# Optimization experiments

Measured on AMD Instinct MI355X. Metric: run time of the kernel, lower is better.

The kernel has to match this reference:

```python
import jax, jax.numpy as jnp
import numpy as np

N, E, F, H = 50000, 400000, 128, 512


def setup_inputs() -> dict:
    key = jax.random.key(0)
    k1, k2, k3 = jax.random.split(key, 3)
    x = jax.random.normal(k1, (N, F), dtype=jnp.float32)
    edge_index = jax.random.randint(k2, (2, E), 0, N, dtype=jnp.int64)
    W = jax.random.normal(k3, (H, F), dtype=jnp.float32) * 0.05  # GCNConv linear weight [out, in]
    b = jnp.zeros((H,), dtype=jnp.float32)
    alpha = jnp.full((H,), 0.25, dtype=jnp.float32)  # PReLU default init per channel
    return {"x": x, "edge_index": edge_index, "W": W, "b": b, "alpha": alpha}


def reference(x, edge_index, W, b, alpha):
    n = x.shape[0]
    # GCNConv: linear transform first (no bias inside the matmul)
    h = x @ W.T  # [N, H]
    # add self-loops (GCNConv default add_self_loops=True)
    loops = jnp.arange(n, dtype=edge_index.dtype)
    row = jnp.concatenate([edge_index[0], loops])  # source
    col = jnp.concatenate([edge_index[1], loops])  # target
    # symmetric degree normalization: deg from edge weights (all ones) summed at targets
    deg = jax.ops.segment_sum(jnp.ones_like(col, dtype=h.dtype), col, num_segments=n)
    dinv = jnp.where(deg > 0, jax.lax.rsqrt(jnp.maximum(deg, 1.0)) * (deg > 0), 0.0)
    dinv = jnp.where(deg > 0, 1.0 / jnp.sqrt(jnp.maximum(deg, 1e-12)), 0.0)
    norm = dinv[row] * dinv[col]  # [E+N]
    # gather source features, scale, scatter-add to targets
    msgs = h[row] * norm[:, None]  # [E+N, H] -- the memory-bound gather
    out = jax.ops.segment_sum(msgs, col, num_segments=n) + b  # [N, H]
    # PReLU with per-channel alpha
    return jnp.where(out > 0, out, alpha * out)
```

## Files before the change

kernel.cpp:

```cpp
#include <hip/hip_runtime.h>


#define F_IN 128
#define H_OUT 512

typedef __bf16 bf16x8 __attribute__((ext_vector_type(8)));
typedef float  f32x4  __attribute__((ext_vector_type(4)));

__global__ __launch_bounds__(256) void prep_kernel(const float* __restrict__ W,
                                                   __bf16* __restrict__ Wb, int nw8,
                                                   const float* __restrict__ x,
                                                   __bf16* __restrict__ xs, int nx8,
                                                   const int* __restrict__ col,
                                                   unsigned* __restrict__ deg,
                                                   unsigned* __restrict__ pos, int E,
                                                   int NWB, int NXB) {
    const int b = blockIdx.x, t = threadIdx.x;
    if (b < NWB) {
        int i = b * 256 + t;
        if (i >= nw8) return;
        float4 a0 = ((const float4*)W)[i * 2];
        float4 a1 = ((const float4*)W)[i * 2 + 1];
        bf16x8 v;
        v[0] = (__bf16)a0.x; v[1] = (__bf16)a0.y; v[2] = (__bf16)a0.z; v[3] = (__bf16)a0.w;
        v[4] = (__bf16)a1.x; v[5] = (__bf16)a1.y; v[6] = (__bf16)a1.z; v[7] = (__bf16)a1.w;
        ((bf16x8*)Wb)[i] = v;
    } else if (b < NWB + NXB) {
        int i = (b - NWB) * 256 + t;
        if (i >= nx8) return;
        float4 a0 = ((const float4*)x)[i * 2];
        float4 a1 = ((const float4*)x)[i * 2 + 1];
        bf16x8 v;
        v[0] = (__bf16)a0.x; v[1] = (__bf16)a0.y; v[2] = (__bf16)a0.z; v[3] = (__bf16)a0.w;
        v[4] = (__bf16)a1.x; v[5] = (__bf16)a1.y; v[6] = (__bf16)a1.z; v[7] = (__bf16)a1.w;
        ((bf16x8*)xs)[i] = v;
    } else {
        int e = (b - NWB - NXB) * 256 + t;
        if (e < E) pos[e] = atomicAdd(&deg[col[e]], 1u);
    }
}

__global__ __launch_bounds__(256) void assign_kernel(const unsigned* __restrict__ deg,
                                                     unsigned* __restrict__ total,
                                                     int* __restrict__ rowptr,
                                                     float* __restrict__ dinv, int n) {
    const int i = blockIdx.x * 256 + threadIdx.x;
    const int lane = threadIdx.x & 63;
    unsigned d = (i < n) ? deg[i] : 0u;
    unsigned da = (d + 7u) & ~7u;
    unsigned x = da;
    #pragma unroll
    for (int o = 1; o < 64; o <<= 1) {
        unsigned y = __shfl_up(x, (unsigned)o, 64);
        if (lane >= o) x += y;
    }
    unsigned tot = __shfl(x, 63, 64);
    unsigned wb = 0;
    if (lane == 63) wb = atomicAdd(total, tot);
    wb = __shfl(wb, 63, 64);
    if (i < n) {
        rowptr[i] = (int)(wb + x - da);
        dinv[i]   = rsqrtf((float)(d + 1u));
    }
}

__global__ __launch_bounds__(256) void fill_csr_kernel(const int* __restrict__ row,
                                                       const int* __restrict__ col,
                                                       const unsigned* __restrict__ pos,
                                                       const int* __restrict__ rowptr,
                                                       int* __restrict__ adj, int E) {
    int e = blockIdx.x * 256 + threadIdx.x;
    if (e >= E) return;
    adj[rowptr[col[e]] + (int)pos[e]] = row[e];
}

__global__ __launch_bounds__(256) void fused_agg_gemm_kernel(
        const int* __restrict__ rowptr, const unsigned* __restrict__ deg,
        const int* __restrict__ adj, const __bf16* __restrict__ xs,
        const float* __restrict__ dinv, const __bf16* __restrict__ Wb,
        const float* __restrict__ bias, const float* __restrict__ alpha,
        float* __restrict__ out, int N) {
    __shared__ __bf16 As[128][136];
    __shared__ __bf16 Bs[128][136];

    const int rb = blockIdx.x * 128;
    const int t  = threadIdx.x;
    const int li   = t & 15;
    const int slot = t >> 4;

    const bf16x8* xs8 = (const bf16x8*)xs;

    for (int nl = slot; nl < 128; nl += 16) {
        const int node = rb + nl;
        bf16x8 o;
        if (node < N) {
            const float dvn = dinv[node];
            bf16x8 sv = xs8[(size_t)node * 16 + li];
            float acc[8];
            #pragma unroll
            for (int q = 0; q < 8; ++q) acc[q] = dvn * (float)sv[q];

            const int s = rowptr[node];
            const int e = s + (int)deg[node];
            for (int j = s; j < e; j += 8) {
                int4 ra = *(const int4*)(adj + j);
                int4 rb4 = *(const int4*)(adj + j + 4);
                int rr[8];
                rr[0] = ra.x;  rr[1] = ra.y;  rr[2] = ra.z;  rr[3] = ra.w;
                rr[4] = rb4.x; rr[5] = rb4.y; rr[6] = rb4.z; rr[7] = rb4.w;
                float wgt[8]; bf16x8 v[8];
                #pragma unroll
                for (int u = 0; u < 8; ++u) {
                    const bool ok = (j + u) < e;
                    const int r = ok ? rr[u] : node;
                    wgt[u] = ok ? dinv[r] : 0.0f;
                    v[u]   = xs8[(size_t)r * 16 + li];
                }
                #pragma unroll
                for (int u = 0; u < 8; ++u) {
                    #pragma unroll
                    for (int q = 0; q < 8; ++q) acc[q] += wgt[u] * (float)v[u][q];
                }
            }
            #pragma unroll
            for (int q = 0; q < 8; ++q) o[q] = (__bf16)(acc[q] * dvn);
        } else {
            #pragma unroll
            for (int q = 0; q < 8; ++q) o[q] = (__bf16)0.0f;
        }
        *(bf16x8*)&As[nl][li * 8] = o;
    }
    __syncthreads();

    const int w    = t >> 6;
    const int lane = t & 63;
    const int lrow = lane & 15;
    const int lk   = (lane >> 4) * 8;
    const int rloc = (lane >> 4) * 4;

    bf16x8 af0[4], af1[4];
    #pragma unroll
    for (int ks = 0; ks < 4; ++ks) {
        const int k0 = ks * 32 + lk;
        af0[ks] = *(const bf16x8*)&As[w * 32 + lrow][k0];
        af1[ks] = *(const bf16x8*)&As[w * 32 + 16 + lrow][k0];
    }

    for (int ct = 0; ct < 4; ++ct) {
        const int cb = ct * 128;
        __syncthreads();
        #pragma unroll
        for (int i = 0; i < 8; ++i) {
            int c  = i * 256 + t;
            int r  = c >> 4;
            int k8 = (c & 15) * 8;
            bf16x8 v = *(const bf16x8*)(Wb + (size_t)(cb + r) * F_IN + k8);
            *(bf16x8*)&Bs[r][k8] = v;
        }
        __syncthreads();

        f32x4 acc[2][8] = {};
        #pragma unroll
        for (int ks = 0; ks < 4; ++ks) {
            const int k0 = ks * 32 + lk;
            #pragma unroll
            for (int tn = 0; tn < 8; ++tn) {
                bf16x8 bfr = *(const bf16x8*)&Bs[tn * 16 + lrow][k0];
                acc[0][tn] = __builtin_amdgcn_mfma_f32_16x16x32_bf16(af0[ks], bfr, acc[0][tn], 0, 0, 0);
                acc[1][tn] = __builtin_amdgcn_mfma_f32_16x16x32_bf16(af1[ks], bfr, acc[1][tn], 0, 0, 0);
            }
        }

        float bb[8], aa[8];
        #pragma unroll
        for (int tn = 0; tn < 8; ++tn) {
            int n = cb + tn * 16 + lrow;
            bb[tn] = bias[n];
            aa[tn] = alpha[n];
        }
        #pragma unroll
        for (int tm = 0; tm < 2; ++tm) {
            #pragma unroll
            for (int r = 0; r < 4; ++r) {
                int m = rb + w * 32 + tm * 16 + rloc + r;
                if (m >= N) continue;
                #pragma unroll
                for (int tn = 0; tn < 8; ++tn) {
                    int n = cb + tn * 16 + lrow;
                    float v = acc[tm][tn][r] + bb[tn];
                    v = v > 0.f ? v : aa[tn] * v;
                    out[(size_t)m * H_OUT + n] = v;
                }
            }
        }
    }
}

extern "C" void kernel_launch(void* const* d_in, const int* in_sizes, int n_in,
                              void* d_out, int out_size, void* d_ws, size_t ws_size,
                              hipStream_t stream) {
    const float* x     = (const float*)d_in[0];
    const int*   ei    = (const int*)d_in[1];
    const float* W     = (const float*)d_in[2];
    const float* b     = (const float*)d_in[3];
    const float* alpha = (const float*)d_in[4];
    float*       out   = (float*)d_out;

    const int N = in_sizes[0] / F_IN;
    const int E = in_sizes[1] / 2;
    const int* row = ei;
    const int* col = ei + E;

    char* wsb = (char*)d_ws;
    size_t off = 0;
    __bf16* xs = (__bf16*)(wsb + off);  off += (size_t)N * F_IN * 2;     off = (off + 63) & ~(size_t)63;
    __bf16* Wb = (__bf16*)(wsb + off);  off += (size_t)H_OUT * F_IN * 2; off = (off + 63) & ~(size_t)63;
    unsigned* deg    = (unsigned*)(wsb + off);  off += (size_t)(N + 1) * 4;
    float*    dinv   = (float*)(wsb + off);     off += (size_t)N * 4;
    int*      rowptr = (int*)(wsb + off);       off += (size_t)N * 4;
    off = (off + 63) & ~(size_t)63;
    unsigned* pos = (unsigned*)(wsb + off);     off += (size_t)E * 4;
    off = (off + 63) & ~(size_t)63;
    int* adj = (int*)(wsb + off);
    unsigned* total = deg + N;

    const int nw8 = H_OUT * F_IN / 8;
    const int nx8 = N * F_IN / 8;
    const int NWB = (nw8 + 255) / 256;
    const int NXB = (nx8 + 255) / 256;
    const int NEB = (E + 255) / 256;

    hipMemsetAsync(deg, 0, (size_t)(N + 1) * 4, stream);
    prep_kernel<<<NWB + NXB + NEB, 256, 0, stream>>>(W, Wb, nw8, x, xs, nx8,
                                                     col, deg, pos, E, NWB, NXB);
    assign_kernel<<<(N + 255) / 256, 256, 0, stream>>>(deg, total, rowptr, dinv, N);
    fill_csr_kernel<<<(E + 255) / 256, 256, 0, stream>>>(row, col, pos, rowptr, adj, E);
    fused_agg_gemm_kernel<<<(N + 127) / 128, 256, 0, stream>>>(
        rowptr, deg, adj, xs, dinv, Wb, b, alpha, out, N);
}
```

Before: 213.3 us.

## Shrink fused agg-GEMM tile to 64 rows, drop LDS weight staging

Halves the rows per block in the fused aggregation+GEMM kernel to 64, launching twice as many blocks. It removes the shared-memory B tile, so weight fragments are read straight from global memory (L2-resident), and that removes the per-column-tile barriers. It also adds a launch bound of 3 blocks per SM and unrolls the loops, all aimed at higher occupancy to hide gather latency. The trade-off is redundant global/L2 weight reads per wave and less MFMA reuse of each B fragment.

```diff
diff --git a/kernel.cpp b/kernel.cpp
--- a/kernel.cpp
+++ b/kernel.cpp
@@ -74,23 +74,23 @@
     adj[rowptr[col[e]] + (int)pos[e]] = row[e];
 }
 
-__global__ __launch_bounds__(256) void fused_agg_gemm_kernel(
+__global__ __launch_bounds__(256, 3) void fused_agg_gemm_kernel(
         const int* __restrict__ rowptr, const unsigned* __restrict__ deg,
         const int* __restrict__ adj, const __bf16* __restrict__ xs,
         const float* __restrict__ dinv, const __bf16* __restrict__ Wb,
         const float* __restrict__ bias, const float* __restrict__ alpha,
         float* __restrict__ out, int N) {
-    __shared__ __bf16 As[128][136];
-    __shared__ __bf16 Bs[128][136];
-
-    const int rb = blockIdx.x * 128;
+    __shared__ __bf16 As[64][136];
+
+    const int rb = blockIdx.x * 64;
     const int t  = threadIdx.x;
     const int li   = t & 15;
     const int slot = t >> 4;
 
     const bf16x8* xs8 = (const bf16x8*)xs;
 
-    for (int nl = slot; nl < 128; nl += 16) {
+    #pragma unroll
+    for (int nl = slot; nl < 64; nl += 16) {
         const int node = rb + nl;
         bf16x8 o;
         if (node < N) {
@@ -103,7 +103,7 @@
             const int s = rowptr[node];
             const int e = s + (int)deg[node];
             for (int j = s; j < e; j += 8) {
-                int4 ra = *(const int4*)(adj + j);
+                int4 ra  = *(const int4*)(adj + j);
                 int4 rb4 = *(const int4*)(adj + j + 4);
                 int rr[8];
                 rr[0] = ra.x;  rr[1] = ra.y;  rr[2] = ra.z;  rr[3] = ra.w;
@@ -138,36 +138,23 @@
     const int lk   = (lane >> 4) * 8;
     const int rloc = (lane >> 4) * 4;
 
-    bf16x8 af0[4], af1[4];
-    #pragma unroll
-    for (int ks = 0; ks < 4; ++ks) {
-        const int k0 = ks * 32 + lk;
-        af0[ks] = *(const bf16x8*)&As[w * 32 + lrow][k0];
-        af1[ks] = *(const bf16x8*)&As[w * 32 + 16 + lrow][k0];
-    }
-
+    bf16x8 af[4];
+    #pragma unroll
+    for (int ks = 0; ks < 4; ++ks)
+        af[ks] = *(const bf16x8*)&As[w * 16 + lrow][ks * 32 + lk];
+
+    #pragma unroll
     for (int ct = 0; ct < 4; ++ct) {
         const int cb = ct * 128;
-        __syncthreads();
-        #pragma unroll
-        for (int i = 0; i < 8; ++i) {
-            int c  = i * 256 + t;
-            int r  = c >> 4;
-            int k8 = (c & 15) * 8;
-            bf16x8 v = *(const bf16x8*)(Wb + (size_t)(cb + r) * F_IN + k8);
-            *(bf16x8*)&Bs[r][k8] = v;
-        }
-        __syncthreads();
-
-        f32x4 acc[2][8] = {};
+
+        f32x4 acc[8] = {};
         #pragma unroll
         for (int ks = 0; ks < 4; ++ks) {
             const int k0 = ks * 32 + lk;
             #pragma unroll
             for (int tn = 0; tn < 8; ++tn) {
-                bf16x8 bfr = *(const bf16x8*)&Bs[tn * 16 + lrow][k0];
-                acc[0][tn] = __builtin_amdgcn_mfma_f32_16x16x32_bf16(af0[ks], bfr, acc[0][tn], 0, 0, 0);
-                acc[1][tn] = __builtin_amdgcn_mfma_f32_16x16x32_bf16(af1[ks], bfr, acc[1][tn], 0, 0, 0);
+                bf16x8 bfr = *(const bf16x8*)(Wb + (size_t)(cb + tn * 16 + lrow) * F_IN + k0);
+                acc[tn] = __builtin_amdgcn_mfma_f32_16x16x32_bf16(af[ks], bfr, acc[tn], 0, 0, 0);
             }
         }
 
@@ -179,18 +166,15 @@
             aa[tn] = alpha[n];
         }
         #pragma unroll
-        for (int tm = 0; tm < 2; ++tm) {
-            #pragma unroll
-            for (int r = 0; r < 4; ++r) {
-                int m = rb + w * 32 + tm * 16 + rloc + r;
-                if (m >= N) continue;
-                #pragma unroll
-                for (int tn = 0; tn < 8; ++tn) {
-                    int n = cb + tn * 16 + lrow;
-                    float v = acc[tm][tn][r] + bb[tn];
-                    v = v > 0.f ? v : aa[tn] * v;
-                    out[(size_t)m * H_OUT + n] = v;
-                }
+        for (int r = 0; r < 4; ++r) {
+            int m = rb + w * 16 + rloc + r;
+            if (m >= N) continue;
+            #pragma unroll
+            for (int tn = 0; tn < 8; ++tn) {
+                int n = cb + tn * 16 + lrow;
+                float v = acc[tn][r] + bb[tn];
+                v = v > 0.f ? v : aa[tn] * v;
+                out[(size_t)m * H_OUT + n] = v;
             }
         }
     }
@@ -235,6 +219,6 @@
                                                      col, deg, pos, E, NWB, NXB);
     assign_kernel<<<(N + 255) / 256, 256, 0, stream>>>(deg, total, rowptr, dinv, N);
     fill_csr_kernel<<<(E + 255) / 256, 256, 0, stream>>>(row, col, pos, rowptr, adj, E);
-    fused_agg_gemm_kernel<<<(N + 127) / 128, 256, 0, stream>>>(
+    fused_agg_gemm_kernel<<<(N + 63) / 64, 256, 0, stream>>>(
         rowptr, deg, adj, xs, dinv, Wb, b, alpha, out, N);
 }
```

Result: slower. 246.8 us (+15.7%).

## Split gather and GEMM into producer/consumer blocks with atomic flag handoff

Applied to the files above, without the earlier changes.

The fused kernel is split into many small gather blocks (16 nodes each) that write aggregated bf16 features to a global buffer, followed by GEMM blocks that spin on per-128-row completion counters before running MFMA. The goal is finer-grained parallelism for the irregular gather and overlap between gather and GEMM phases inside one launch. The GEMM now uses 64-column W tiles with smaller LDS, launch_bounds occupancy 4, and nontemporal output stores. It adds a global round trip for aggregated features and relies on dispatch order for the spin-wait to avoid deadlock.

```diff
diff --git a/kernel.cpp b/kernel.cpp
--- a/kernel.cpp
+++ b/kernel.cpp
@@ -74,26 +74,23 @@
     adj[rowptr[col[e]] + (int)pos[e]] = row[e];
 }
 
-__global__ __launch_bounds__(256) void fused_agg_gemm_kernel(
+__global__ __launch_bounds__(256, 4) void gather_gemm_kernel(
         const int* __restrict__ rowptr, const unsigned* __restrict__ deg,
         const int* __restrict__ adj, const __bf16* __restrict__ xs,
-        const float* __restrict__ dinv, const __bf16* __restrict__ Wb,
-        const float* __restrict__ bias, const float* __restrict__ alpha,
-        float* __restrict__ out, int N) {
-    __shared__ __bf16 As[128][136];
-    __shared__ __bf16 Bs[128][136];
-
-    const int rb = blockIdx.x * 128;
-    const int t  = threadIdx.x;
-    const int li   = t & 15;
-    const int slot = t >> 4;
-
-    const bf16x8* xs8 = (const bf16x8*)xs;
-
-    for (int nl = slot; nl < 128; nl += 16) {
-        const int node = rb + nl;
-        bf16x8 o;
+        const float* __restrict__ dinv, __bf16* __restrict__ ag,
+        const __bf16* __restrict__ Wb, const float* __restrict__ bias,
+        const float* __restrict__ alpha, unsigned* __restrict__ done,
+        float* __restrict__ out, int N, int NGB) {
+    __shared__ __bf16 Bs[64][136];
+
+    const int bid = blockIdx.x;
+    const int t   = threadIdx.x;
+
+    if (bid < NGB) {
+        const int node = bid * 16 + (t >> 4);
+        const int li   = t & 15;
         if (node < N) {
+            const bf16x8* xs8 = (const bf16x8*)xs;
             const float dvn = dinv[node];
             bf16x8 sv = xs8[(size_t)node * 16 + li];
             float acc[8];
@@ -103,7 +100,7 @@
             const int s = rowptr[node];
             const int e = s + (int)deg[node];
             for (int j = s; j < e; j += 8) {
-                int4 ra = *(const int4*)(adj + j);
+                int4 ra  = *(const int4*)(adj + j);
                 int4 rb4 = *(const int4*)(adj + j + 4);
                 int rr[8];
                 rr[0] = ra.x;  rr[1] = ra.y;  rr[2] = ra.z;  rr[3] = ra.w;
@@ -122,58 +119,86 @@
                     for (int q = 0; q < 8; ++q) acc[q] += wgt[u] * (float)v[u][q];
                 }
             }
+
+            bf16x8 o;
             #pragma unroll
             for (int q = 0; q < 8; ++q) o[q] = (__bf16)(acc[q] * dvn);
-        } else {
-            #pragma unroll
-            for (int q = 0; q < 8; ++q) o[q] = (__bf16)0.0f;
-        }
-        *(bf16x8*)&As[nl][li * 8] = o;
+            ((bf16x8*)ag)[(size_t)node * 16 + li] = o;
+        }
+        __syncthreads();
+        if (t == 0)
+            __hip_atomic_fetch_add(&done[bid >> 3], 1u,
+                                   __ATOMIC_RELEASE, __HIP_MEMORY_SCOPE_AGENT);
+        return;
+    }
+
+    const int rbi = bid - NGB;
+    const int rb  = rbi * 128;
+
+    #pragma unroll
+    for (int i = 0; i < 4; ++i) {
+        int c  = i * 256 + t;
+        int r  = c >> 4;
+        int k8 = (c & 15) * 8;
+        *(bf16x8*)&Bs[r][k8] = *(const bf16x8*)(Wb + (size_t)r * F_IN + k8);
+    }
+
+    const int nprod = NGB - rbi * 8;
+    const int expct = nprod < 8 ? nprod : 8;
+    if (t == 0) {
+        while ((int)__hip_atomic_load(&done[rbi], __ATOMIC_ACQUIRE,
+                                      __HIP_MEMORY_SCOPE_AGENT) < expct)
+            __builtin_amdgcn_s_sleep(2);
     }
     __syncthreads();
 
     const int w    = t >> 6;
     const int lane = t & 63;
     const int lrow = lane & 15;
-    const int lk   = (lane >> 4) * 8;
+    const int lkc  = lane >> 4;
     const int rloc = (lane >> 4) * 4;
 
+    const bf16x8* ag8 = (const bf16x8*)ag;
+    int r0 = rb + w * 32 + lrow;      if (r0 > N - 1) r0 = N - 1;
+    int r1 = rb + w * 32 + 16 + lrow; if (r1 > N - 1) r1 = N - 1;
     bf16x8 af0[4], af1[4];
     #pragma unroll
     for (int ks = 0; ks < 4; ++ks) {
-        const int k0 = ks * 32 + lk;
-        af0[ks] = *(const bf16x8*)&As[w * 32 + lrow][k0];
-        af1[ks] = *(const bf16x8*)&As[w * 32 + 16 + lrow][k0];
-    }
-
-    for (int ct = 0; ct < 4; ++ct) {
-        const int cb = ct * 128;
-        __syncthreads();
-        #pragma unroll
-        for (int i = 0; i < 8; ++i) {
-            int c  = i * 256 + t;
-            int r  = c >> 4;
-            int k8 = (c & 15) * 8;
-            bf16x8 v = *(const bf16x8*)(Wb + (size_t)(cb + r) * F_IN + k8);
-            *(bf16x8*)&Bs[r][k8] = v;
-        }
-        __syncthreads();
-
-        f32x4 acc[2][8] = {};
+        af0[ks] = ag8[(size_t)r0 * 16 + ks * 4 + lkc];
+        af1[ks] = ag8[(size_t)r1 * 16 + ks * 4 + lkc];
+    }
+
+    #pragma unroll
+    for (int ct = 0; ct < 8; ++ct) {
+        const int cb = ct * 64;
+        if (ct) {
+            __syncthreads();
+            #pragma unroll
+            for (int i = 0; i < 4; ++i) {
+                int c  = i * 256 + t;
+                int r  = c >> 4;
+                int k8 = (c & 15) * 8;
+                *(bf16x8*)&Bs[r][k8] =
+                    *(const bf16x8*)(Wb + (size_t)(cb + r) * F_IN + k8);
+            }
+            __syncthreads();
+        }
+
+        f32x4 acc[2][4] = {};
         #pragma unroll
         for (int ks = 0; ks < 4; ++ks) {
-            const int k0 = ks * 32 + lk;
-            #pragma unroll
-            for (int tn = 0; tn < 8; ++tn) {
+            const int k0 = ks * 32 + lkc * 8;
+            #pragma unroll
+            for (int tn = 0; tn < 4; ++tn) {
                 bf16x8 bfr = *(const bf16x8*)&Bs[tn * 16 + lrow][k0];
                 acc[0][tn] = __builtin_amdgcn_mfma_f32_16x16x32_bf16(af0[ks], bfr, acc[0][tn], 0, 0, 0);
                 acc[1][tn] = __builtin_amdgcn_mfma_f32_16x16x32_bf16(af1[ks], bfr, acc[1][tn], 0, 0, 0);
             }
         }
 
-        float bb[8], aa[8];
+        float bb[4], aa[4];
         #pragma unroll
-        for (int tn = 0; tn < 8; ++tn) {
+        for (int tn = 0; tn < 4; ++tn) {
             int n = cb + tn * 16 + lrow;
             bb[tn] = bias[n];
             aa[tn] = alpha[n];
@@ -185,11 +210,11 @@
                 int m = rb + w * 32 + tm * 16 + rloc + r;
                 if (m >= N) continue;
                 #pragma unroll
-                for (int tn = 0; tn < 8; ++tn) {
+                for (int tn = 0; tn < 4; ++tn) {
                     int n = cb + tn * 16 + lrow;
                     float v = acc[tm][tn][r] + bb[tn];
                     v = v > 0.f ? v : aa[tn] * v;
-                    out[(size_t)m * H_OUT + n] = v;
+                    __builtin_nontemporal_store(v, &out[(size_t)m * H_OUT + n]);
                 }
             }
         }
@@ -211,15 +236,20 @@
     const int* row = ei;
     const int* col = ei + E;
 
+    const int NGB = (N + 15) / 16;
+    const int NRB = (N + 127) / 128;
+
     char* wsb = (char*)d_ws;
     size_t off = 0;
     __bf16* xs = (__bf16*)(wsb + off);  off += (size_t)N * F_IN * 2;     off = (off + 63) & ~(size_t)63;
+    __bf16* ag = (__bf16*)(wsb + off);  off += (size_t)N * F_IN * 2;     off = (off + 63) & ~(size_t)63;
     __bf16* Wb = (__bf16*)(wsb + off);  off += (size_t)H_OUT * F_IN * 2; off = (off + 63) & ~(size_t)63;
-    unsigned* deg    = (unsigned*)(wsb + off);  off += (size_t)(N + 1) * 4;
-    float*    dinv   = (float*)(wsb + off);     off += (size_t)N * 4;
-    int*      rowptr = (int*)(wsb + off);       off += (size_t)N * 4;
+    unsigned* deg  = (unsigned*)(wsb + off);  off += (size_t)(N + 1) * 4;
+    unsigned* done = (unsigned*)(wsb + off);  off += (size_t)NRB * 4;
+    float*    dinv   = (float*)(wsb + off);   off += (size_t)N * 4;
+    int*      rowptr = (int*)(wsb + off);     off += (size_t)N * 4;
     off = (off + 63) & ~(size_t)63;
-    unsigned* pos = (unsigned*)(wsb + off);     off += (size_t)E * 4;
+    unsigned* pos = (unsigned*)(wsb + off);   off += (size_t)E * 4;
     off = (off + 63) & ~(size_t)63;
     int* adj = (int*)(wsb + off);
     unsigned* total = deg + N;
@@ -230,11 +260,11 @@
     const int NXB = (nx8 + 255) / 256;
     const int NEB = (E + 255) / 256;
 
-    hipMemsetAsync(deg, 0, (size_t)(N + 1) * 4, stream);
+    hipMemsetAsync(deg, 0, (size_t)(N + 1 + NRB) * 4, stream);
     prep_kernel<<<NWB + NXB + NEB, 256, 0, stream>>>(W, Wb, nw8, x, xs, nx8,
                                                      col, deg, pos, E, NWB, NXB);
     assign_kernel<<<(N + 255) / 256, 256, 0, stream>>>(deg, total, rowptr, dinv, N);
     fill_csr_kernel<<<(E + 255) / 256, 256, 0, stream>>>(row, col, pos, rowptr, adj, E);
-    fused_agg_gemm_kernel<<<(N + 127) / 128, 256, 0, stream>>>(
-        rowptr, deg, adj, xs, dinv, Wb, b, alpha, out, N);
-}
+    gather_gemm_kernel<<<NGB + NRB, 256, 0, stream>>>(
+        rowptr, deg, adj, xs, dinv, ag, Wb, b, alpha, done, out, N, NGB);
+}
```

Measured after the change: 288.4 us. 1.35x slower.
